# Kernel optimization log

Hardware: AMD Instinct MI355X
Metric: run time of the kernel (lower is better)

## Reference

```python
import jax, jax.numpy as jnp
import numpy as np

N_NODES = 50000
N_EDGES = 600000
LATENT = 128
STEPS = 4
BN_EPS = 1e-5


def _bn(h, gamma, beta):
    # BatchNorm1d in training mode: batch statistics over the row dim (biased var)
    mean = jnp.mean(h, axis=0)
    var = jnp.var(h, axis=0)
    return gamma * (h - mean) * jax.lax.rsqrt(var + BN_EPS) + beta


def setup_inputs() -> dict:
    key = jax.random.key(0)
    ks = jax.random.split(key, 9)
    L, S = LATENT, STEPS
    d = {}
    d["x"] = jax.random.normal(ks[0], (N_NODES, L), dtype=jnp.float32)
    d["edge_attr"] = jax.random.normal(ks[1], (N_EDGES, L), dtype=jnp.float32)
    d["edge_index"] = jax.random.randint(ks[2], (2, N_EDGES), 0, N_NODES, dtype=jnp.int64)
    # MLP weights: small init (BN normalizes hidden activations anyway)
    d["edge_W1"] = jax.random.normal(ks[3], (S, 3 * L, L), dtype=jnp.float32) * (1.0 / np.sqrt(3 * L))
    d["edge_b1"] = jnp.zeros((S, L), jnp.float32)
    d["edge_g1"] = jnp.ones((S, L), jnp.float32)
    d["edge_be1"] = jnp.zeros((S, L), jnp.float32)
    d["edge_W2"] = jax.random.normal(ks[4], (S, L, L), dtype=jnp.float32) * (1.0 / np.sqrt(L))
    d["edge_b2"] = jnp.zeros((S, L), jnp.float32)
    d["node_W1"] = jax.random.normal(ks[5], (S, 2 * L, L), dtype=jnp.float32) * (1.0 / np.sqrt(2 * L))
    d["node_b1"] = jnp.zeros((S, L), jnp.float32)
    d["node_g1"] = jnp.ones((S, L), jnp.float32)
    d["node_be1"] = jnp.zeros((S, L), jnp.float32)
    d["node_W2"] = jax.random.normal(ks[6], (S, L, L), dtype=jnp.float32) * (1.0 / np.sqrt(L))
    d["node_b2"] = jnp.zeros((S, L), jnp.float32)
    return d


def reference(x, edge_attr, edge_index, edge_W1, edge_b1, edge_g1, edge_be1,
              edge_W2, edge_b2, node_W1, node_b1, node_g1, node_be1,
              node_W2, node_b2):
    src = edge_index[0]  # x_j (source)
    dst = edge_index[1]  # x_i (target), also the scatter target
    for s in range(STEPS):
        # --- edge update (message) ---
        m = jnp.concatenate([x[dst], x[src], edge_attr], axis=1)  # [E, 3L]
        h = _bn(m @ edge_W1[s] + edge_b1[s], edge_g1[s], edge_be1[s])
        h = jax.nn.relu(h)
        h = jax.nn.relu(h @ edge_W2[s] + edge_b2[s])
        edge_attr = h + edge_attr  # residual
        # --- aggregate: scatter-sum to target nodes ---
        agg = jax.ops.segment_sum(edge_attr, dst, num_segments=N_NODES)  # [N, L]
        # --- node update ---
        n = jnp.concatenate([x, agg], axis=1)  # [N, 2L]
        h = _bn(n @ node_W1[s] + node_b1[s], node_g1[s], node_be1[s])
        h = jax.nn.relu(h)
        h = jax.nn.relu(h @ node_W2[s] + node_b2[s])
        x = h + x  # residual
    return x, edge_attr
```

## Files before the change

kernel.cpp:

```cpp
#include <hip/hip_runtime.h>
#include <hip/hip_bf16.h>
#include <cstdint>
#include <cstddef>

#define E_N 600000
#define NND 50000
#define L 128
#define EGRID 4688
#define PBLK 16384

typedef unsigned short u16;
typedef unsigned int u32;
typedef __attribute__((ext_vector_type(8))) short bf16x8;
typedef __attribute__((ext_vector_type(4))) float f32x4;

static __device__ __forceinline__ u16 f2bf(float f) {
  union { float f; u32 u; } c; c.f = f;
  return (u16)((c.u + 0x7fffu + ((c.u >> 16) & 1u)) >> 16);
}
static __device__ __forceinline__ u32 pk2(float a, float b) {
  return (u32)f2bf(a) | ((u32)f2bf(b) << 16);
}
static __device__ __forceinline__ float bf2f(u32 h) {
  union { u32 u; float f; } c; c.u = (h & 0xffffu) << 16; return c.f;
}
static __device__ __forceinline__ void atomAddF(float* p, float v) {
#if defined(__HIP_DEVICE_COMPILE__)
  unsafeAtomicAdd(p, v);
#else
  atomicAdd(p, v);
#endif
}
static __device__ __forceinline__ bf16x8 bnrelu8(bf16x8 raw, float4 sca, float4 scb,
                                                 float4 sha, float4 shb) {
  union { bf16x8 v; u16 h[8]; } in; in.v = raw;
  const float sc[8] = {sca.x, sca.y, sca.z, sca.w, scb.x, scb.y, scb.z, scb.w};
  const float sh[8] = {sha.x, sha.y, sha.z, sha.w, shb.x, shb.y, shb.z, shb.w};
  float f[8];
  #pragma unroll
  for (int i = 0; i < 8; ++i) f[i] = fmaxf(bf2f(in.h[i]) * sc[i] + sh[i], 0.f);
  union { bf16x8 v; u32 w[4]; } r;
  #pragma unroll
  for (int i = 0; i < 4; ++i) r.w[i] = pk2(f[2 * i], f[2 * i + 1]);
  return r.v;
}

#define MFMA(a, bfr, c) __builtin_amdgcn_mfma_f32_16x16x32_bf16((a), (bfr), (c), 0, 0, 0)

static __device__ __forceinline__ size_t paddr(int row, int panel, int incol) {
  return (size_t)(row >> 7) * PBLK + (size_t)panel * 2048 + (size_t)(row & 127) * 16 + incol;
}

__global__ __launch_bounds__(256) void k_cvt4(const float* __restrict__ in,
                                              u16* __restrict__ out, int n4) {
  const int i = blockIdx.x * 256 + threadIdx.x;
  if (i < n4) {
    const float4 v = *(const float4*)(in + (size_t)i * 4);
    uint2 o; o.x = pk2(v.x, v.y); o.y = pk2(v.z, v.w);
    *(uint2*)(out + (size_t)i * 4) = o;
  }
}

__global__ void k_wt(const float* __restrict__ W, u16* __restrict__ Wt, int K) {
  const int idx = blockIdx.x * 256 + threadIdx.x;
  const int total = 4 * K * 128;
  if (idx >= total) return;
  const int s = idx / (K * 128);
  const int rem = idx - s * K * 128;
  const int n = rem / K;
  const int k = rem - n * K;
  Wt[idx] = f2bf(W[(size_t)s * K * 128 + (size_t)k * 128 + n]);
}

__global__ void k_hist(const int* __restrict__ dstI, int* __restrict__ cnt) {
  const int i = blockIdx.x * 256 + threadIdx.x;
  if (i < E_N) atomicAdd(&cnt[dstI[i]], 1);
}

__global__ __launch_bounds__(1024) void k_scan(const int* __restrict__ cnt, int* __restrict__ startA) {
  __shared__ int buf[1024];
  __shared__ int carry;
  const int tid = threadIdx.x;
  if (tid == 0) carry = 0;
  __syncthreads();
  for (int base = 0; base < NND; base += 1024) {
    int v = (base + tid < NND) ? cnt[base + tid] : 0;
    buf[tid] = v;
    __syncthreads();
    for (int off = 1; off < 1024; off <<= 1) {
      int t = (tid >= off) ? buf[tid - off] : 0;
      __syncthreads();
      buf[tid] += t;
      __syncthreads();
    }
    const int incl = buf[tid];
    const int c = carry;
    if (base + tid < NND) startA[base + tid] = c + incl - v;
    __syncthreads();
    if (tid == 1023) carry = c + incl;
    __syncthreads();
  }
  if (tid == 0) startA[NND] = carry;
}

__global__ void k_fill(const int* __restrict__ dstI, const int* __restrict__ startA,
                       int* __restrict__ cur, int* __restrict__ eids) {
  const int i = blockIdx.x * 256 + threadIdx.x;
  if (i < E_N) {
    const int d = dstI[i];
    const int pos = atomicAdd(&cur[d], 1);
    eids[startA[d] + pos] = i;
  }
}

__global__ void k_perm(const int* __restrict__ srcI, const int* __restrict__ dstI,
                       const int* __restrict__ perm,
                       int* __restrict__ srcP, int* __restrict__ dstP) {
  const int i = blockIdx.x * 256 + threadIdx.x;
  if (i < E_N) {
    const int e = perm[i];
    srcP[i] = srcI[e];
    dstP[i] = dstI[e];
  }
}

__global__ __launch_bounds__(256) void k_agg(const u16* __restrict__ ea16,
                                             const int* __restrict__ startA,
                                             u16* __restrict__ agg16) {
  const int node = blockIdx.x * 4 + (threadIdx.x >> 6);
  const int lane = threadIdx.x & 63;
  if (node >= NND) return;
  const int s = startA[node], e = startA[node + 1];
  const size_t poff = (size_t)(lane >> 3) * 2048 + (size_t)((lane & 7) * 2);
  float a0 = 0.f, a1 = 0.f, b0 = 0.f, b1 = 0.f;
  int i = s;
  for (; i + 1 < e; i += 2) {
    const u32 v0 = *(const u32*)(ea16 + (size_t)(i >> 7) * PBLK + (size_t)(i & 127) * 16 + poff);
    const int j = i + 1;
    const u32 v1 = *(const u32*)(ea16 + (size_t)(j >> 7) * PBLK + (size_t)(j & 127) * 16 + poff);
    a0 += bf2f(v0); a1 += bf2f(v0 >> 16);
    b0 += bf2f(v1); b1 += bf2f(v1 >> 16);
  }
  if (i < e) {
    const u32 v = *(const u32*)(ea16 + (size_t)(i >> 7) * PBLK + (size_t)(i & 127) * 16 + poff);
    a0 += bf2f(v); a1 += bf2f(v >> 16);
  }
  *(u32*)(agg16 + (size_t)node * L + lane * 2) = pk2(a0 + b0, a1 + b1);
}

__global__ void k_bnfin(const float* __restrict__ gS, const float* __restrict__ g,
                        const float* __restrict__ be, float invM, float* __restrict__ ss) {
  const int c = threadIdx.x;
  float s1 = 0.f, s2 = 0.f;
  for (int j = 0; j < 64; ++j) { s1 += gS[j * L + c]; s2 += gS[64 * L + j * L + c]; }
  const float mean = s1 * invM;
  const float var = s2 * invM - mean * mean;
  const float sc = g[c] * rsqrtf(var + 1e-5f);
  ss[c] = sc;
  ss[L + c] = be[c] - mean * sc;
}

template <bool EA32>
__global__ __launch_bounds__(512, 3) void k_edge_l1(
    const u16* __restrict__ x16, const float* __restrict__ ea32,
    const u16* __restrict__ ea16, const int* __restrict__ perm,
    const int* __restrict__ srcP, const int* __restrict__ dstP,
    const u16* __restrict__ Wt, const float* __restrict__ b,
    u16* __restrict__ h1, float* __restrict__ gS)
{
  __shared__ __align__(16) char AsB[3 * 16384];
  __shared__ float red[256];
  const int tid = threadIdx.x, bid = blockIdx.x, row0 = bid * 128;
  const int lane = tid & 63, wid = tid >> 6;
  const int l15 = lane & 15, lq = lane >> 4;
  const int col = wid * 16 + l15;

  const int kcMap[6] = {4, 5, 0, 1, 2, 3};
  bf16x8 Bf[12];
  #pragma unroll
  for (int cc = 0; cc < 6; ++cc)
    #pragma unroll
    for (int k2 = 0; k2 < 2; ++k2)
      Bf[cc * 2 + k2] = *(const bf16x8*)(Wt + (size_t)col * 384 + kcMap[cc] * 64 + k2 * 32 + lq * 8);

  const int srow = tid >> 2, spart = tid & 3;
  const int crow = min(row0 + srow, E_N - 1);
  const int sd = dstP[crow], ssr = srcP[crow];
  const int prow = EA32 ? perm[crow] : 0;

  f32x4 acc[8];
  #pragma unroll
  for (int m = 0; m < 8; ++m) acc[m] = (f32x4){0.f, 0.f, 0.f, 0.f};

  uint4 ra[2], rb[2];
  auto sload = [&](int cc, uint4* v) {
    if (cc >= 2) {
      const int node = (cc >= 4) ? ssr : sd;
      const u16* p = x16 + (size_t)node * L + (cc & 1) * 64 + spart * 16;
      v[0] = *(const uint4*)p; v[1] = *(const uint4*)(p + 8);
    } else if (EA32) {
      const float* p = ea32 + (size_t)prow * L + cc * 64 + spart * 16;
      const float4 f0 = *(const float4*)p,       f1 = *(const float4*)(p + 4);
      const float4 f2 = *(const float4*)(p + 8), f3 = *(const float4*)(p + 12);
      v[0].x = pk2(f0.x, f0.y); v[0].y = pk2(f0.z, f0.w);
      v[0].z = pk2(f1.x, f1.y); v[0].w = pk2(f1.z, f1.w);
      v[1].x = pk2(f2.x, f2.y); v[1].y = pk2(f2.z, f2.w);
      v[1].z = pk2(f3.x, f3.y); v[1].w = pk2(f3.z, f3.w);
    } else {
      const u16* p = ea16 + paddr(crow, cc * 4 + spart, 0);
      v[0] = *(const uint4*)p; v[1] = *(const uint4*)(p + 8);
    }
  };
  auto swrite = [&](int buf, const uint4* v) {
    char* base = AsB + buf * 16384;
    const int sw = (srow & 7) << 4;
    const int b0 = srow * 128 + spart * 32;
    *(uint4*)(base + (b0 ^ sw)) = v[0];
    *(uint4*)(base + ((b0 + 16) ^ sw)) = v[1];
  };

  sload(0, ra); sload(1, rb);
  swrite(0, ra);
  __syncthreads();
  #pragma unroll
  for (int cc = 0; cc < 6; ++cc) {
    if (cc + 2 < 6) sload(cc + 2, (cc & 1) ? rb : ra);
    if (cc + 1 < 6) swrite((cc + 1) % 3, (cc & 1) ? ra : rb);
    const char* base = AsB + (cc % 3) * 16384;
    #pragma unroll
    for (int m = 0; m < 8; ++m) {
      const int row = m * 16 + l15;
      const int sw = (row & 7) << 4;
      #pragma unroll
      for (int k2 = 0; k2 < 2; ++k2) {
        const bf16x8 af = *(const bf16x8*)(base + ((row * 128 + k2 * 64 + lq * 16) ^ sw));
        acc[m] = MFMA(Bf[cc * 2 + k2], af, acc[m]);
      }
    }
    __syncthreads();
  }

  const int colb = wid * 16 + lq * 4;
  float bb[4];
  #pragma unroll
  for (int r = 0; r < 4; ++r) bb[r] = b[colb + r];
  float s1[4] = {0.f, 0.f, 0.f, 0.f}, s2[4] = {0.f, 0.f, 0.f, 0.f};
  u16* hp = h1 + (size_t)bid * PBLK + (size_t)wid * 2048 + lq * 4;
  #pragma unroll
  for (int m = 0; m < 8; ++m) {
    const int rl = m * 16 + l15;
    if (row0 + rl < E_N) {
      ushort4 st;
      float o0 = acc[m][0] + bb[0], o1 = acc[m][1] + bb[1];
      float o2 = acc[m][2] + bb[2], o3 = acc[m][3] + bb[3];
      s1[0] += o0; s2[0] += o0 * o0; s1[1] += o1; s2[1] += o1 * o1;
      s1[2] += o2; s2[2] += o2 * o2; s1[3] += o3; s2[3] += o3 * o3;
      st.x = f2bf(o0); st.y = f2bf(o1); st.z = f2bf(o2); st.w = f2bf(o3);
      *(ushort4*)(hp + rl * 16) = st;
    }
  }
  #pragma unroll
  for (int off = 1; off < 16; off <<= 1) {
    #pragma unroll
    for (int r = 0; r < 4; ++r) {
      s1[r] += __shfl_xor(s1[r], off);
      s2[r] += __shfl_xor(s2[r], off);
    }
  }
  if (l15 == 0) {
    float4 v1; v1.x = s1[0]; v1.y = s1[1]; v1.z = s1[2]; v1.w = s1[3];
    float4 v2; v2.x = s2[0]; v2.y = s2[1]; v2.z = s2[2]; v2.w = s2[3];
    *(float4*)(&red[colb]) = v1;
    *(float4*)(&red[128 + colb]) = v2;
  }
  __syncthreads();
  const int slot = (bid & 63) * L;
  if (tid < 128) atomAddF(&gS[slot + tid], red[tid]);
  else if (tid < 256) atomAddF(&gS[64 * L + slot + (tid - 128)], red[tid]);
}

template <bool EA32, bool WF32>
__global__ __launch_bounds__(512, 4) void k_edge_l2(
    const u16* __restrict__ h1, const float* __restrict__ ss,
    const u16* __restrict__ Wt, const float* __restrict__ b,
    const float* __restrict__ resid32, const u16* __restrict__ resid16,
    const int* __restrict__ perm,
    float* __restrict__ ea_out, u16* __restrict__ ea16)
{
  __shared__ __align__(16) char AsB[2 * 16384];
  const int tid = threadIdx.x, bid = blockIdx.x, row0 = bid * 128;
  const int lane = tid & 63, wid = tid >> 6;
  const int l15 = lane & 15, lq = lane >> 4;
  const int col = wid * 16 + l15;

  bf16x8 Bf[4];
  #pragma unroll
  for (int k = 0; k < 4; ++k)
    Bf[k] = *(const bf16x8*)(Wt + (size_t)col * 128 + k * 32 + lq * 8);

  const int srow = tid >> 2, spart = tid & 3;
  const int crow = min(row0 + srow, E_N - 1);

  #pragma unroll
  for (int cc = 0; cc < 2; ++cc) {
    const int kb = cc * 64 + spart * 16;
    const float4 c0 = *(const float4*)(ss + kb),      c1 = *(const float4*)(ss + kb + 4);
    const float4 c2 = *(const float4*)(ss + kb + 8),  c3 = *(const float4*)(ss + kb + 12);
    const float4 g0 = *(const float4*)(ss + 128 + kb),     g1 = *(const float4*)(ss + 128 + kb + 4);
    const float4 g2 = *(const float4*)(ss + 128 + kb + 8), g3 = *(const float4*)(ss + 128 + kb + 12);
    const u16* p = h1 + paddr(crow, cc * 4 + spart, 0);
    bf16x8 r0 = *(const bf16x8*)p, r1 = *(const bf16x8*)(p + 8);
    r0 = bnrelu8(r0, c0, c1, g0, g1);
    r1 = bnrelu8(r1, c2, c3, g2, g3);
    char* base = AsB + cc * 16384;
    const int sw = (srow & 7) << 4;
    const int b0 = srow * 128 + spart * 32;
    *(bf16x8*)(base + (b0 ^ sw)) = r0;
    *(bf16x8*)(base + ((b0 + 16) ^ sw)) = r1;
  }
  __syncthreads();

  f32x4 acc[8];
  #pragma unroll
  for (int m = 0; m < 8; ++m) acc[m] = (f32x4){0.f, 0.f, 0.f, 0.f};
  #pragma unroll
  for (int cc = 0; cc < 2; ++cc) {
    const char* base = AsB + cc * 16384;
    #pragma unroll
    for (int m = 0; m < 8; ++m) {
      const int row = m * 16 + l15;
      const int sw = (row & 7) << 4;
      #pragma unroll
      for (int k2 = 0; k2 < 2; ++k2) {
        const bf16x8 af = *(const bf16x8*)(base + ((row * 128 + k2 * 64 + lq * 16) ^ sw));
        acc[m] = MFMA(Bf[cc * 2 + k2], af, acc[m]);
      }
    }
  }

  const int colb = wid * 16 + lq * 4;
  float bb[4];
  #pragma unroll
  for (int r = 0; r < 4; ++r) bb[r] = b[colb + r];
  u16* ep = ea16 + (size_t)bid * PBLK + (size_t)wid * 2048 + lq * 4;
  #pragma unroll
  for (int m = 0; m < 8; ++m) {
    const int rl = m * 16 + l15;
    const int row = row0 + rl;
    if (row < E_N) {
      float o[4];
      #pragma unroll
      for (int r = 0; r < 4; ++r) o[r] = fmaxf(acc[m][r] + bb[r], 0.f);
      if (EA32) {
        const float4 rv = *(const float4*)(resid32 + (size_t)perm[row] * L + colb);
        o[0] += rv.x; o[1] += rv.y; o[2] += rv.z; o[3] += rv.w;
      } else {
        const ushort4 rv = *(const ushort4*)(resid16 + (size_t)bid * PBLK + (size_t)wid * 2048 + rl * 16 + lq * 4);
        o[0] += bf2f(rv.x); o[1] += bf2f(rv.y); o[2] += bf2f(rv.z); o[3] += bf2f(rv.w);
      }
      ushort4 st;
      st.x = f2bf(o[0]); st.y = f2bf(o[1]); st.z = f2bf(o[2]); st.w = f2bf(o[3]);
      *(ushort4*)(ep + rl * 16) = st;
      if (WF32) {
        float4 fv; fv.x = o[0]; fv.y = o[1]; fv.z = o[2]; fv.w = o[3];
        *(float4*)(ea_out + (size_t)perm[row] * L + colb) = fv;
      }
    }
  }
}

__global__ __launch_bounds__(256) void k_node_l1(
    const u16* __restrict__ x16, const u16* __restrict__ agg16,
    const u16* __restrict__ Wt, const float* __restrict__ b,
    u16* __restrict__ h1, float* __restrict__ gS)
{
  __shared__ __align__(16) char Bs[2][16384];
  __shared__ float red[256];
  const int tid = threadIdx.x, bid = blockIdx.x, row0 = bid * 64;
  red[tid] = 0.f;
  const int lane = tid & 63, wid = tid >> 6, wr = wid >> 1, wc = wid & 1;
  const int l15 = lane & 15, lq = lane >> 4;
  const int r0 = row0 + wr * 32 + l15, r1 = r0 + 16;
  const int rr0 = min(r0, NND - 1), rr1 = min(r1, NND - 1);

  const u16* aP[2][2];
  aP[0][0] = x16 + (size_t)rr0 * L;   aP[1][0] = x16 + (size_t)rr1 * L;
  aP[0][1] = agg16 + (size_t)rr0 * L; aP[1][1] = agg16 + (size_t)rr1 * L;

  f32x4 acc[2][4];
  #pragma unroll
  for (int m = 0; m < 2; ++m)
    #pragma unroll
    for (int n = 0; n < 4; ++n) acc[m][n] = (f32x4){0.f, 0.f, 0.f, 0.f};

  auto loadA = [&](int c, bf16x8 (&af)[2][2]) {
    const int seg = c >> 1;
    const int base = (c & 1) * 64 + lq * 8;
    #pragma unroll
    for (int k2 = 0; k2 < 2; ++k2) {
      af[0][k2] = *(const bf16x8*)(aP[0][seg] + base + k2 * 32);
      af[1][k2] = *(const bf16x8*)(aP[1][seg] + base + k2 * 32);
    }
  };
  auto stage = [&](int c, int buf) {
    #pragma unroll
    for (int i = 0; i < 4; ++i) {
      const int slot = tid + i * 256;
      const int n = slot >> 3, kq = slot & 7;
      const uint4 v = *(const uint4*)(Wt + (size_t)n * 256 + c * 64 + kq * 8);
      *(uint4*)(&Bs[buf][0] + ((n * 128 + kq * 16) ^ ((n & 7) << 4))) = v;
    }
  };

  bf16x8 aCur[2][2], aNxt[2][2];
  loadA(0, aCur);
  stage(0, 0);
  __syncthreads();
  #pragma unroll
  for (int c = 0; c < 4; ++c) {
    if (c + 1 < 4) loadA(c + 1, aNxt);
    {
      const char* base = &Bs[c & 1][0];
      #pragma unroll
      for (int k2 = 0; k2 < 2; ++k2)
        #pragma unroll
        for (int n = 0; n < 4; ++n) {
          const int ncol = wc * 64 + n * 16 + l15;
          const bf16x8 bfr = *(const bf16x8*)(base + ((ncol * 128 + k2 * 64 + lq * 16) ^ ((ncol & 7) << 4)));
          acc[0][n] = MFMA(aCur[0][k2], bfr, acc[0][n]);
          acc[1][n] = MFMA(aCur[1][k2], bfr, acc[1][n]);
        }
    }
    if (c + 1 < 4) stage(c + 1, (c + 1) & 1);
    __syncthreads();
    #pragma unroll
    for (int m = 0; m < 2; ++m)
      #pragma unroll
      for (int k2 = 0; k2 < 2; ++k2) aCur[m][k2] = aNxt[m][k2];
  }

  float bb[4], s1[4], s2[4];
  #pragma unroll
  for (int n = 0; n < 4; ++n) { bb[n] = b[wc * 64 + n * 16 + l15]; s1[n] = 0.f; s2[n] = 0.f; }
  #pragma unroll
  for (int m = 0; m < 2; ++m)
    #pragma unroll
    for (int n = 0; n < 4; ++n) {
      const int ncol = wc * 64 + n * 16 + l15;
      #pragma unroll
      for (int r = 0; r < 4; ++r) {
        const int row = row0 + wr * 32 + m * 16 + lq * 4 + r;
        if (row < NND) {
          const float o = acc[m][n][r] + bb[n];
          s1[n] += o; s2[n] += o * o;
          h1[(size_t)row * L + ncol] = f2bf(o);
        }
      }
    }
  #pragma unroll
  for (int n = 0; n < 4; ++n) {
    const int ncol = wc * 64 + n * 16 + l15;
    atomAddF(&red[ncol], s1[n]);
    atomAddF(&red[128 + ncol], s2[n]);
  }
  __syncthreads();
  const int slot = (bid & 63) * L;
  if (tid < 128) atomAddF(&gS[slot + tid], red[tid]);
  else atomAddF(&gS[64 * L + slot + (tid - 128)], red[tid]);
}

__global__ __launch_bounds__(256) void k_node_l2(
    const u16* __restrict__ h1, const float* __restrict__ ss,
    const u16* __restrict__ Wt, const float* __restrict__ b,
    const float* __restrict__ resid, float* __restrict__ x_out,
    u16* __restrict__ x16)
{
  __shared__ __align__(16) char Bs[2][16384];
  const int tid = threadIdx.x, bid = blockIdx.x, row0 = bid * 64;
  const int lane = tid & 63, wid = tid >> 6, wr = wid >> 1, wc = wid & 1;
  const int l15 = lane & 15, lq = lane >> 4;
  const int r0 = row0 + wr * 32 + l15, r1 = r0 + 16;
  const int rr0 = min(r0, NND - 1), rr1 = min(r1, NND - 1);
  const u16* a0 = h1 + (size_t)rr0 * L + lq * 8;
  const u16* a1 = h1 + (size_t)rr1 * L + lq * 8;

  f32x4 acc[2][4];
  #pragma unroll
  for (int m = 0; m < 2; ++m)
    #pragma unroll
    for (int n = 0; n < 4; ++n) acc[m][n] = (f32x4){0.f, 0.f, 0.f, 0.f};

  auto stage = [&](int c, int buf) {
    #pragma unroll
    for (int i = 0; i < 4; ++i) {
      const int slot = tid + i * 256;
      const int n = slot >> 3, kq = slot & 7;
      const uint4 v = *(const uint4*)(Wt + (size_t)n * 128 + c * 64 + kq * 8);
      *(uint4*)(&Bs[buf][0] + ((n * 128 + kq * 16) ^ ((n & 7) << 4))) = v;
    }
  };
  stage(0, 0);
  stage(1, 1);
  bf16x8 raw[2][2][2];
  #pragma unroll
  for (int c = 0; c < 2; ++c)
    #pragma unroll
    for (int k2 = 0; k2 < 2; ++k2) {
      raw[c][0][k2] = *(const bf16x8*)(a0 + c * 64 + k2 * 32);
      raw[c][1][k2] = *(const bf16x8*)(a1 + c * 64 + k2 * 32);
    }
  __syncthreads();

  #pragma unroll
  for (int c = 0; c < 2; ++c) {
    bf16x8 af[2][2];
    #pragma unroll
    for (int k2 = 0; k2 < 2; ++k2) {
      const int kg = c * 64 + k2 * 32 + lq * 8;
      const float4 sca = *(const float4*)(ss + kg), scb = *(const float4*)(ss + kg + 4);
      const float4 sha = *(const float4*)(ss + 128 + kg), shb = *(const float4*)(ss + 128 + kg + 4);
      af[0][k2] = bnrelu8(raw[c][0][k2], sca, scb, sha, shb);
      af[1][k2] = bnrelu8(raw[c][1][k2], sca, scb, sha, shb);
    }
    const char* base = &Bs[c][0];
    #pragma unroll
    for (int k2 = 0; k2 < 2; ++k2)
      #pragma unroll
      for (int n = 0; n < 4; ++n) {
        const int ncol = wc * 64 + n * 16 + l15;
        const bf16x8 bfr = *(const bf16x8*)(base + ((ncol * 128 + k2 * 64 + lq * 16) ^ ((ncol & 7) << 4)));
        acc[0][n] = MFMA(af[0][k2], bfr, acc[0][n]);
        acc[1][n] = MFMA(af[1][k2], bfr, acc[1][n]);
      }
  }

  float bb[4];
  #pragma unroll
  for (int n = 0; n < 4; ++n) bb[n] = b[wc * 64 + n * 16 + l15];
  #pragma unroll
  for (int m = 0; m < 2; ++m)
    #pragma unroll
    for (int n = 0; n < 4; ++n) {
      const int ncol = wc * 64 + n * 16 + l15;
      #pragma unroll
      for (int r = 0; r < 4; ++r) {
        const int row = row0 + wr * 32 + m * 16 + lq * 4 + r;
        if (row < NND) {
          const float o = fmaxf(acc[m][n][r] + bb[n], 0.f) + resid[(size_t)row * L + ncol];
          x_out[(size_t)row * L + ncol] = o;
          x16[(size_t)row * L + ncol] = f2bf(o);
        }
      }
    }
}

extern "C" void kernel_launch(void* const* d_in, const int* in_sizes, int n_in,
                              void* d_out, int out_size, void* d_ws, size_t ws_size,
                              hipStream_t stream) {
  (void)in_sizes; (void)n_in; (void)out_size; (void)ws_size;
  const float* in_x  = (const float*)d_in[0];
  const float* in_ea = (const float*)d_in[1];
  const int*   ei    = (const int*)d_in[2];
  const float* eW1 = (const float*)d_in[3];
  const float* eb1 = (const float*)d_in[4];
  const float* eg1 = (const float*)d_in[5];
  const float* ebe1= (const float*)d_in[6];
  const float* eW2 = (const float*)d_in[7];
  const float* eb2 = (const float*)d_in[8];
  const float* nW1 = (const float*)d_in[9];
  const float* nb1 = (const float*)d_in[10];
  const float* ng1 = (const float*)d_in[11];
  const float* nbe1= (const float*)d_in[12];
  const float* nW2 = (const float*)d_in[13];
  const float* nb2 = (const float*)d_in[14];

  float* x  = (float*)d_out;
  float* ea = (float*)d_out + (size_t)NND * L;

  char* w = (char*)d_ws;
  u16* h1e   = (u16*)w;   w += (size_t)EGRID * PBLK * sizeof(u16);
  u16* ea16  = (u16*)w;   w += (size_t)EGRID * PBLK * sizeof(u16);
  u16* h1n   = (u16*)w;   w += (size_t)NND * L * sizeof(u16);
  u16* x16   = (u16*)w;   w += (size_t)NND * L * sizeof(u16);
  u16* agg16 = (u16*)w;   w += (size_t)NND * L * sizeof(u16);
  float* gS  = (float*)w; w += (size_t)2 * 64 * L * sizeof(float);
  float* ss  = (float*)w; w += 4096;
  u16* eW1t = (u16*)w;   w += (size_t)4 * 128 * 384 * sizeof(u16);
  u16* eW2t = (u16*)w;   w += (size_t)4 * 128 * 128 * sizeof(u16);
  u16* nW1t = (u16*)w;   w += (size_t)4 * 128 * 256 * sizeof(u16);
  u16* nW2t = (u16*)w;   w += (size_t)4 * 128 * 128 * sizeof(u16);
  int* cnt    = (int*)w; w += (size_t)NND * sizeof(int);
  int* cur    = (int*)w; w += (size_t)NND * sizeof(int);
  int* startA = (int*)w; w += (size_t)(NND + 64) * sizeof(int);
  int* eids   = (int*)w; w += (size_t)E_N * sizeof(int);
  int* srcP   = (int*)w; w += (size_t)E_N * sizeof(int);
  int* dstP   = (int*)w; w += (size_t)E_N * sizeof(int);

  const int* srcI = ei;
  const int* dstI = ei + E_N;

  k_cvt4<<<(NND * L / 4 + 255) / 256, 256, 0, stream>>>(in_x, x16, NND * L / 4);
  k_wt<<<(4 * 384 * 128 + 255) / 256, 256, 0, stream>>>(eW1, eW1t, 384);
  k_wt<<<(4 * 128 * 128 + 255) / 256, 256, 0, stream>>>(eW2, eW2t, 128);
  k_wt<<<(4 * 256 * 128 + 255) / 256, 256, 0, stream>>>(nW1, nW1t, 256);
  k_wt<<<(4 * 128 * 128 + 255) / 256, 256, 0, stream>>>(nW2, nW2t, 128);
  hipMemsetAsync(cnt, 0, (size_t)NND * sizeof(int), stream);
  hipMemsetAsync(cur, 0, (size_t)NND * sizeof(int), stream);
  k_hist<<<(E_N + 255) / 256, 256, 0, stream>>>(dstI, cnt);
  k_scan<<<1, 1024, 0, stream>>>(cnt, startA);
  k_fill<<<(E_N + 255) / 256, 256, 0, stream>>>(dstI, startA, cur, eids);
  k_perm<<<(E_N + 255) / 256, 256, 0, stream>>>(srcI, dstI, eids, srcP, dstP);

  const int ngrid = (NND + 63) / 64;

  for (int s = 0; s < 4; ++s) {
    hipMemsetAsync(gS, 0, (size_t)2 * 64 * L * sizeof(float), stream);
    if (s == 0)
      k_edge_l1<true><<<EGRID, 512, 0, stream>>>(x16, in_ea, nullptr, eids, srcP, dstP,
          eW1t + (size_t)s * 128 * 384, eb1 + (size_t)s * L, h1e, gS);
    else
      k_edge_l1<false><<<EGRID, 512, 0, stream>>>(x16, nullptr, ea16, eids, srcP, dstP,
          eW1t + (size_t)s * 128 * 384, eb1 + (size_t)s * L, h1e, gS);
    k_bnfin<<<1, 128, 0, stream>>>(gS, eg1 + (size_t)s * L, ebe1 + (size_t)s * L,
        1.f / (float)E_N, ss);
    if (s == 0)
      k_edge_l2<true, false><<<EGRID, 512, 0, stream>>>(h1e, ss,
          eW2t + (size_t)s * 128 * 128, eb2 + (size_t)s * L, in_ea, nullptr, eids, ea, ea16);
    else if (s < 3)
      k_edge_l2<false, false><<<EGRID, 512, 0, stream>>>(h1e, ss,
          eW2t + (size_t)s * 128 * 128, eb2 + (size_t)s * L, nullptr, ea16, eids, ea, ea16);
    else
      k_edge_l2<false, true><<<EGRID, 512, 0, stream>>>(h1e, ss,
          eW2t + (size_t)s * 128 * 128, eb2 + (size_t)s * L, nullptr, ea16, eids, ea, ea16);
    k_agg<<<(NND + 3) / 4, 256, 0, stream>>>(ea16, startA, agg16);
    hipMemsetAsync(gS, 0, (size_t)2 * 64 * L * sizeof(float), stream);
    k_node_l1<<<ngrid, 256, 0, stream>>>(x16, agg16,
        nW1t + (size_t)s * 128 * 256, nb1 + (size_t)s * L, h1n, gS);
    k_bnfin<<<1, 128, 0, stream>>>(gS, ng1 + (size_t)s * L, nbe1 + (size_t)s * L,
        1.f / (float)NND, ss);
    k_node_l2<<<ngrid, 256, 0, stream>>>(h1n, ss,
        nW2t + (size_t)s * 128 * 128, nb2 + (size_t)s * L,
        (s == 0) ? in_x : x, x, x16);
  }
}
```

Measured before the change: 2.183 ms.

## Load edge MLP operands straight from global into MFMA registers, drop LDS staging

```diff
diff --git a/kernel.cpp b/kernel.cpp
--- a/kernel.cpp
+++ b/kernel.cpp
@@ -58,6 +58,21 @@
     const float4 v = *(const float4*)(in + (size_t)i * 4);
     uint2 o; o.x = pk2(v.x, v.y); o.y = pk2(v.z, v.w);
     *(uint2*)(out + (size_t)i * 4) = o;
+  }
+}
+
+__global__ __launch_bounds__(256) void k_cvtperm(const float* __restrict__ in_ea,
+                                                 const int* __restrict__ perm,
+                                                 u16* __restrict__ ea16) {
+  const int i = blockIdx.x * 256 + threadIdx.x;
+  const int row = i >> 4, part = i & 15;
+  if (row < E_N) {
+    const float* p = in_ea + (size_t)perm[row] * L + part * 8;
+    const float4 f0 = *(const float4*)p, f1 = *(const float4*)(p + 4);
+    union { bf16x8 v; u32 w[4]; } r;
+    r.w[0] = pk2(f0.x, f0.y); r.w[1] = pk2(f0.z, f0.w);
+    r.w[2] = pk2(f1.x, f1.y); r.w[3] = pk2(f1.z, f1.w);
+    *(bf16x8*)(ea16 + paddr(row, part >> 1, (part & 1) * 8)) = r.v;
   }
 }
 
@@ -160,84 +175,55 @@
   ss[L + c] = be[c] - mean * sc;
 }
 
-template <bool EA32>
-__global__ __launch_bounds__(512, 3) void k_edge_l1(
-    const u16* __restrict__ x16, const float* __restrict__ ea32,
-    const u16* __restrict__ ea16, const int* __restrict__ perm,
+__global__ __launch_bounds__(512, 4) void k_edge_l1(
+    const u16* __restrict__ x16, const u16* __restrict__ ea16,
     const int* __restrict__ srcP, const int* __restrict__ dstP,
     const u16* __restrict__ Wt, const float* __restrict__ b,
     u16* __restrict__ h1, float* __restrict__ gS)
 {
-  __shared__ __align__(16) char AsB[3 * 16384];
   __shared__ float red[256];
   const int tid = threadIdx.x, bid = blockIdx.x, row0 = bid * 128;
   const int lane = tid & 63, wid = tid >> 6;
   const int l15 = lane & 15, lq = lane >> 4;
   const int col = wid * 16 + l15;
 
-  const int kcMap[6] = {4, 5, 0, 1, 2, 3};
   bf16x8 Bf[12];
   #pragma unroll
   for (int cc = 0; cc < 6; ++cc)
     #pragma unroll
     for (int k2 = 0; k2 < 2; ++k2)
-      Bf[cc * 2 + k2] = *(const bf16x8*)(Wt + (size_t)col * 384 + kcMap[cc] * 64 + k2 * 32 + lq * 8);
-
-  const int srow = tid >> 2, spart = tid & 3;
-  const int crow = min(row0 + srow, E_N - 1);
-  const int sd = dstP[crow], ssr = srcP[crow];
-  const int prow = EA32 ? perm[crow] : 0;
+      Bf[cc * 2 + k2] = *(const bf16x8*)(Wt + (size_t)col * 384 + cc * 64 + k2 * 32 + lq * 8);
+
+  int dIdx[8], sIdx[8], crw[8];
+  #pragma unroll
+  for (int m = 0; m < 8; ++m) {
+    crw[m] = min(row0 + m * 16 + l15, E_N - 1);
+    dIdx[m] = dstP[crw[m]];
+    sIdx[m] = srcP[crw[m]];
+  }
 
   f32x4 acc[8];
   #pragma unroll
   for (int m = 0; m < 8; ++m) acc[m] = (f32x4){0.f, 0.f, 0.f, 0.f};
 
-  uint4 ra[2], rb[2];
-  auto sload = [&](int cc, uint4* v) {
-    if (cc >= 2) {
-      const int node = (cc >= 4) ? ssr : sd;
-      const u16* p = x16 + (size_t)node * L + (cc & 1) * 64 + spart * 16;
-      v[0] = *(const uint4*)p; v[1] = *(const uint4*)(p + 8);
-    } else if (EA32) {
-      const float* p = ea32 + (size_t)prow * L + cc * 64 + spart * 16;
-      const float4 f0 = *(const float4*)p,       f1 = *(const float4*)(p + 4);
-      const float4 f2 = *(const float4*)(p + 8), f3 = *(const float4*)(p + 12);
-      v[0].x = pk2(f0.x, f0.y); v[0].y = pk2(f0.z, f0.w);
-      v[0].z = pk2(f1.x, f1.y); v[0].w = pk2(f1.z, f1.w);
-      v[1].x = pk2(f2.x, f2.y); v[1].y = pk2(f2.z, f2.w);
-      v[1].z = pk2(f3.x, f3.y); v[1].w = pk2(f3.z, f3.w);
-    } else {
-      const u16* p = ea16 + paddr(crow, cc * 4 + spart, 0);
-      v[0] = *(const uint4*)p; v[1] = *(const uint4*)(p + 8);
-    }
-  };
-  auto swrite = [&](int buf, const uint4* v) {
-    char* base = AsB + buf * 16384;
-    const int sw = (srow & 7) << 4;
-    const int b0 = srow * 128 + spart * 32;
-    *(uint4*)(base + (b0 ^ sw)) = v[0];
-    *(uint4*)(base + ((b0 + 16) ^ sw)) = v[1];
-  };
-
-  sload(0, ra); sload(1, rb);
-  swrite(0, ra);
-  __syncthreads();
   #pragma unroll
   for (int cc = 0; cc < 6; ++cc) {
-    if (cc + 2 < 6) sload(cc + 2, (cc & 1) ? rb : ra);
-    if (cc + 1 < 6) swrite((cc + 1) % 3, (cc & 1) ? ra : rb);
-    const char* base = AsB + (cc % 3) * 16384;
     #pragma unroll
     for (int m = 0; m < 8; ++m) {
-      const int row = m * 16 + l15;
-      const int sw = (row & 7) << 4;
-      #pragma unroll
-      for (int k2 = 0; k2 < 2; ++k2) {
-        const bf16x8 af = *(const bf16x8*)(base + ((row * 128 + k2 * 64 + lq * 16) ^ sw));
-        acc[m] = MFMA(Bf[cc * 2 + k2], af, acc[m]);
+      bf16x8 af0, af1;
+      if (cc < 4) {
+        const int node = (cc < 2) ? dIdx[m] : sIdx[m];
+        const u16* p = x16 + (size_t)node * L + (cc & 1) * 64 + lq * 8;
+        af0 = *(const bf16x8*)p;
+        af1 = *(const bf16x8*)(p + 32);
+      } else {
+        const int pc = cc - 4;
+        af0 = *(const bf16x8*)(ea16 + paddr(crw[m], pc * 4 + (lq >> 1), (lq & 1) * 8));
+        af1 = *(const bf16x8*)(ea16 + paddr(crw[m], pc * 4 + 2 + (lq >> 1), (lq & 1) * 8));
       }
-    }
-    __syncthreads();
+      acc[m] = MFMA(Bf[cc * 2 + 0], af0, acc[m]);
+      acc[m] = MFMA(Bf[cc * 2 + 1], af1, acc[m]);
+    }
   }
 
   const int colb = wid * 16 + lq * 4;
@@ -279,15 +265,13 @@
   else if (tid < 256) atomAddF(&gS[64 * L + slot + (tid - 128)], red[tid]);
 }
 
-template <bool EA32, bool WF32>
+template <bool WF32>
 __global__ __launch_bounds__(512, 4) void k_edge_l2(
     const u16* __restrict__ h1, const float* __restrict__ ss,
     const u16* __restrict__ Wt, const float* __restrict__ b,
-    const float* __restrict__ resid32, const u16* __restrict__ resid16,
     const int* __restrict__ perm,
     float* __restrict__ ea_out, u16* __restrict__ ea16)
 {
-  __shared__ __align__(16) char AsB[2 * 16384];
   const int tid = threadIdx.x, bid = blockIdx.x, row0 = bid * 128;
   const int lane = tid & 63, wid = tid >> 6;
   const int l15 = lane & 15, lq = lane >> 4;
@@ -298,45 +282,29 @@
   for (int k = 0; k < 4; ++k)
     Bf[k] = *(const bf16x8*)(Wt + (size_t)col * 128 + k * 32 + lq * 8);
 
-  const int srow = tid >> 2, spart = tid & 3;
-  const int crow = min(row0 + srow, E_N - 1);
-
-  #pragma unroll
-  for (int cc = 0; cc < 2; ++cc) {
-    const int kb = cc * 64 + spart * 16;
-    const float4 c0 = *(const float4*)(ss + kb),      c1 = *(const float4*)(ss + kb + 4);
-    const float4 c2 = *(const float4*)(ss + kb + 8),  c3 = *(const float4*)(ss + kb + 12);
-    const float4 g0 = *(const float4*)(ss + 128 + kb),     g1 = *(const float4*)(ss + 128 + kb + 4);
-    const float4 g2 = *(const float4*)(ss + 128 + kb + 8), g3 = *(const float4*)(ss + 128 + kb + 12);
-    const u16* p = h1 + paddr(crow, cc * 4 + spart, 0);
-    bf16x8 r0 = *(const bf16x8*)p, r1 = *(const bf16x8*)(p + 8);
-    r0 = bnrelu8(r0, c0, c1, g0, g1);
-    r1 = bnrelu8(r1, c2, c3, g2, g3);
-    char* base = AsB + cc * 16384;
-    const int sw = (srow & 7) << 4;
-    const int b0 = srow * 128 + spart * 32;
-    *(bf16x8*)(base + (b0 ^ sw)) = r0;
-    *(bf16x8*)(base + ((b0 + 16) ^ sw)) = r1;
-  }
-  __syncthreads();
+  int crw[8];
+  #pragma unroll
+  for (int m = 0; m < 8; ++m) crw[m] = min(row0 + m * 16 + l15, E_N - 1);
 
   f32x4 acc[8];
   #pragma unroll
   for (int m = 0; m < 8; ++m) acc[m] = (f32x4){0.f, 0.f, 0.f, 0.f};
-  #pragma unroll
-  for (int cc = 0; cc < 2; ++cc) {
-    const char* base = AsB + cc * 16384;
-    #pragma unroll
-    for (int m = 0; m < 8; ++m) {
-      const int row = m * 16 + l15;
-      const int sw = (row & 7) << 4;
+
+  #pragma unroll
+  for (int cc = 0; cc < 2; ++cc)
+    #pragma unroll
+    for (int k2 = 0; k2 < 2; ++k2) {
+      const int kb = cc * 64 + k2 * 32 + lq * 8;
+      const float4 sca = *(const float4*)(ss + kb), scb = *(const float4*)(ss + kb + 4);
+      const float4 sha = *(const float4*)(ss + 128 + kb), shb = *(const float4*)(ss + 128 + kb + 4);
+      const int panel = (kb >> 4);
+      const int incol = kb & 15;
       #pragma unroll
-      for (int k2 = 0; k2 < 2; ++k2) {
-        const bf16x8 af = *(const bf16x8*)(base + ((row * 128 + k2 * 64 + lq * 16) ^ sw));
-        acc[m] = MFMA(Bf[cc * 2 + k2], af, acc[m]);
+      for (int m = 0; m < 8; ++m) {
+        const bf16x8 raw = *(const bf16x8*)(h1 + paddr(crw[m], panel, incol));
+        acc[m] = MFMA(Bf[cc * 2 + k2], bnrelu8(raw, sca, scb, sha, shb), acc[m]);
       }
     }
-  }
 
   const int colb = wid * 16 + lq * 4;
   float bb[4];
@@ -351,13 +319,8 @@
       float o[4];
       #pragma unroll
       for (int r = 0; r < 4; ++r) o[r] = fmaxf(acc[m][r] + bb[r], 0.f);
-      if (EA32) {
-        const float4 rv = *(const float4*)(resid32 + (size_t)perm[row] * L + colb);
-        o[0] += rv.x; o[1] += rv.y; o[2] += rv.z; o[3] += rv.w;
-      } else {
-        const ushort4 rv = *(const ushort4*)(resid16 + (size_t)bid * PBLK + (size_t)wid * 2048 + rl * 16 + lq * 4);
-        o[0] += bf2f(rv.x); o[1] += bf2f(rv.y); o[2] += bf2f(rv.z); o[3] += bf2f(rv.w);
-      }
+      const ushort4 rv = *(const ushort4*)(ep + rl * 16);
+      o[0] += bf2f(rv.x); o[1] += bf2f(rv.y); o[2] += bf2f(rv.z); o[3] += bf2f(rv.w);
       ushort4 st;
       st.x = f2bf(o[0]); st.y = f2bf(o[1]); st.z = f2bf(o[2]); st.w = f2bf(o[3]);
       *(ushort4*)(ep + rl * 16) = st;
@@ -610,28 +573,22 @@
   k_scan<<<1, 1024, 0, stream>>>(cnt, startA);
   k_fill<<<(E_N + 255) / 256, 256, 0, stream>>>(dstI, startA, cur, eids);
   k_perm<<<(E_N + 255) / 256, 256, 0, stream>>>(srcI, dstI, eids, srcP, dstP);
+  k_cvtperm<<<(E_N * 16 + 255) / 256, 256, 0, stream>>>(in_ea, eids, ea16);
 
   const int ngrid = (NND + 63) / 64;
 
   for (int s = 0; s < 4; ++s) {
     hipMemsetAsync(gS, 0, (size_t)2 * 64 * L * sizeof(float), stream);
-    if (s == 0)
-      k_edge_l1<true><<<EGRID, 512, 0, stream>>>(x16, in_ea, nullptr, eids, srcP, dstP,
-          eW1t + (size_t)s * 128 * 384, eb1 + (size_t)s * L, h1e, gS);
-    else
-      k_edge_l1<false><<<EGRID, 512, 0, stream>>>(x16, nullptr, ea16, eids, srcP, dstP,
-          eW1t + (size_t)s * 128 * 384, eb1 + (size_t)s * L, h1e, gS);
+    k_edge_l1<<<EGRID, 512, 0, stream>>>(x16, ea16, srcP, dstP,
+        eW1t + (size_t)s * 128 * 384, eb1 + (size_t)s * L, h1e, gS);
     k_bnfin<<<1, 128, 0, stream>>>(gS, eg1 + (size_t)s * L, ebe1 + (size_t)s * L,
         1.f / (float)E_N, ss);
-    if (s == 0)
-      k_edge_l2<true, false><<<EGRID, 512, 0, stream>>>(h1e, ss,
-          eW2t + (size_t)s * 128 * 128, eb2 + (size_t)s * L, in_ea, nullptr, eids, ea, ea16);
-    else if (s < 3)
-      k_edge_l2<false, false><<<EGRID, 512, 0, stream>>>(h1e, ss,
-          eW2t + (size_t)s * 128 * 128, eb2 + (size_t)s * L, nullptr, ea16, eids, ea, ea16);
+    if (s < 3)
+      k_edge_l2<false><<<EGRID, 512, 0, stream>>>(h1e, ss,
+          eW2t + (size_t)s * 128 * 128, eb2 + (size_t)s * L, eids, ea, ea16);
     else
-      k_edge_l2<false, true><<<EGRID, 512, 0, stream>>>(h1e, ss,
-          eW2t + (size_t)s * 128 * 128, eb2 + (size_t)s * L, nullptr, ea16, eids, ea, ea16);
+      k_edge_l2<true><<<EGRID, 512, 0, stream>>>(h1e, ss,
+          eW2t + (size_t)s * 128 * 128, eb2 + (size_t)s * L, eids, ea, ea16);
     k_agg<<<(NND + 3) / 4, 256, 0, stream>>>(ea16, startA, agg16);
     hipMemsetAsync(gS, 0, (size_t)2 * 64 * L * sizeof(float), stream);
     k_node_l1<<<ngrid, 256, 0, stream>>>(x16, agg16,
```

New measurement: 2.790 ms. 1.28x slower.
